# Performance work log

Measured on AMD Instinct MI355X. Metric: run time of the kernel, lower is better.

Reference implementation:

```python
import jax, jax.numpy as jnp
import numpy as np

B, SQ, SK, D = 8, 4096, 4096, 64


def setup_inputs() -> dict:
    key = jax.random.key(0)
    k1, k2, k3 = jax.random.split(key, 3)
    x1 = jax.random.normal(k1, (B, SQ, D), dtype=jnp.float32)   # queries
    x2 = jax.random.normal(k2, (B, SK, D), dtype=jnp.float32)   # keys
    x3 = jax.random.normal(k3, (B, SK, D), dtype=jnp.float32)   # values
    x4 = 0                                                      # dropout p (static, 0 => deterministic)
    x5 = jnp.ones((1,), dtype=jnp.float32)                      # scale divisor
    return {"x1": x1, "x2": x2, "x3": x3, "x4": x4, "x5": x5}


def reference(x1, x2, x3, x4, x5):
    # scores: [B, Sq, Sk]
    scores = jnp.einsum("bqd,bkd->bqk", x1, x2) / x5
    attn = jax.nn.softmax(scores, axis=-1)
    p = float(x4)  # static python scalar
    if p > 0.0:
        mask = jax.random.bernoulli(jax.random.key(42), 1.0 - p, attn.shape)
        attn = attn * mask.astype(attn.dtype) / (1.0 - p)
    # out: [B, Sq, D]
    return jnp.einsum("bqk,bkd->bqd", attn, x3)
```

## Files before the change

kernel.cpp:

```cpp
#include <hip/hip_runtime.h>


typedef _Float16 f16x8 __attribute__((ext_vector_type(8)));
typedef _Float16 f16x4 __attribute__((ext_vector_type(4)));
typedef __fp16   h16x2 __attribute__((ext_vector_type(2)));
typedef float    f32x4 __attribute__((ext_vector_type(4)));

constexpr int kB  = 8;
constexpr int kSQ = 4096;
constexpr int kSK = 4096;
constexpr int kD  = 64;
constexpr int BQ  = 64;
constexpr int BK  = 64;
constexpr int LDK = kD + 8;
constexpr int LDV = BK + 8;
constexpr int LDP = BK + 8;

static __device__ __forceinline__ f16x4 pack4(float a, float b, float c, float d) {
    h16x2 p0 = __builtin_amdgcn_cvt_pkrtz(a, b);
    h16x2 p1 = __builtin_amdgcn_cvt_pkrtz(c, d);
    f16x4 r;
    r[0] = (_Float16)p0[0]; r[1] = (_Float16)p0[1];
    r[2] = (_Float16)p1[0]; r[3] = (_Float16)p1[1];
    return r;
}

__global__ __launch_bounds__(256, 2)
void fattn_kernel(const float* __restrict__ Qg,
                  const float* __restrict__ Kg,
                  const float* __restrict__ Vg,
                  const float* __restrict__ sdiv,
                  float* __restrict__ Og)
{
    __shared__ __align__(16) _Float16 sK[2][BK][LDK];
    __shared__ __align__(16) _Float16 sV[2][kD][LDV];
    __shared__ __align__(16) _Float16 sP[4][16][LDP];

    const int tid  = threadIdx.x;
    const int w    = tid >> 6;
    const int lane = tid & 63;
    const int l16  = lane & 15;
    const int quad = lane >> 4;

    const int b  = blockIdx.y;
    const int qb = blockIdx.x * BQ;

    const float inv_scale = 1.0f / sdiv[0];

    const float* Qb = Qg + ((size_t)b * kSQ + qb) * kD;
    const float* Kb = Kg + (size_t)b * kSK * kD;
    const float* Vb = Vg + (size_t)b * kSK * kD;

    f16x8 qf[2];
    {
        const float* qrow = Qb + (size_t)(w * 16 + l16) * kD;
#pragma unroll
        for (int ks = 0; ks < 2; ++ks) {
            const float4 a = *(const float4*)(qrow + ks * 32 + quad * 8);
            const float4 c = *(const float4*)(qrow + ks * 32 + quad * 8 + 4);
            f16x4 lo = pack4(a.x * inv_scale, a.y * inv_scale, a.z * inv_scale, a.w * inv_scale);
            f16x4 hi = pack4(c.x * inv_scale, c.y * inv_scale, c.z * inv_scale, c.w * inv_scale);
            f16x8 f;
            f[0] = lo[0]; f[1] = lo[1]; f[2] = lo[2]; f[3] = lo[3];
            f[4] = hi[0]; f[5] = hi[1]; f[6] = hi[2]; f[7] = hi[3];
            qf[ks] = f;
        }
    }

    const int kp0 = 2 * ((0 * 256 + tid) >> 4), cb0 = ((0 * 256 + tid) & 15) * 4;
    const int kp1 = 2 * ((1 * 256 + tid) >> 4), cb1 = ((1 * 256 + tid) & 15) * 4;
    const int kq  = tid >> 4;
    const int fq  = tid & 15;
    const int kqs = (kq ^ (fq & 14)) * 4;

    float4 rk[2][2];
    float4 rv[4];

    auto load_tile = [&](int kt) {
        const float* Kt = Kb + (size_t)kt * BK * kD;
        const float* Vt = Vb + (size_t)kt * BK * kD;
        rk[0][0] = *(const float4*)(Kt + (kp0 + 0) * kD + cb0);
        rk[0][1] = *(const float4*)(Kt + (kp0 + 1) * kD + cb0);
        rk[1][0] = *(const float4*)(Kt + (kp1 + 0) * kD + cb1);
        rk[1][1] = *(const float4*)(Kt + (kp1 + 1) * kD + cb1);
#pragma unroll
        for (int r = 0; r < 4; ++r)
            rv[r] = *(const float4*)(Vt + (4 * kq + r) * kD + 4 * fq);
    };

    auto write_tile = [&](int buf) {
        *(f16x4*)&sK[buf][kp0 + 0][cb0] = pack4(rk[0][0].x, rk[0][0].y, rk[0][0].z, rk[0][0].w);
        *(f16x4*)&sK[buf][kp0 + 1][cb0] = pack4(rk[0][1].x, rk[0][1].y, rk[0][1].z, rk[0][1].w);
        *(f16x4*)&sK[buf][kp1 + 0][cb1] = pack4(rk[1][0].x, rk[1][0].y, rk[1][0].z, rk[1][0].w);
        *(f16x4*)&sK[buf][kp1 + 1][cb1] = pack4(rk[1][1].x, rk[1][1].y, rk[1][1].z, rk[1][1].w);
        const float vx[4][4] = {
            {rv[0].x, rv[0].y, rv[0].z, rv[0].w},
            {rv[1].x, rv[1].y, rv[1].z, rv[1].w},
            {rv[2].x, rv[2].y, rv[2].z, rv[2].w},
            {rv[3].x, rv[3].y, rv[3].z, rv[3].w}};
#pragma unroll
        for (int j = 0; j < 4; ++j)
            *(f16x4*)&sV[buf][4 * fq + j][kqs] =
                pack4(vx[0][j], vx[1][j], vx[2][j], vx[3][j]);
    };

    f32x4 o[4];
    float m_i = -1e30f, l_i = 0.0f;
#pragma unroll
    for (int dt = 0; dt < 4; ++dt)
#pragma unroll
        for (int r = 0; r < 4; ++r) o[dt][r] = 0.0f;

    load_tile(0);
    write_tile(0);
    __syncthreads();

    const int nIter = kSK / BK;
    for (int kt = 0; kt < nIter; ++kt) {
        const int buf = kt & 1;
        const bool more = (kt + 1 < nIter);
        if (more) load_tile(kt + 1);

        f32x4 s[4];
#pragma unroll
        for (int nt = 0; nt < 4; ++nt) {
            const f16x8 kf0 = *(const f16x8*)&sK[buf][nt * 16 + l16][quad * 8];
            const f16x8 kf1 = *(const f16x8*)&sK[buf][nt * 16 + l16][32 + quad * 8];
            f32x4 acc;
#pragma unroll
            for (int r = 0; r < 4; ++r) acc[r] = 0.0f;
            acc = __builtin_amdgcn_mfma_f32_16x16x32_f16(kf0, qf[0], acc, 0, 0, 0);
            acc = __builtin_amdgcn_mfma_f32_16x16x32_f16(kf1, qf[1], acc, 0, 0, 0);
            s[nt] = acc;
        }

        float rm = s[0][0];
#pragma unroll
        for (int nt = 0; nt < 4; ++nt)
#pragma unroll
            for (int r = 0; r < 4; ++r) rm = fmaxf(rm, s[nt][r]);
        rm = fmaxf(rm, __shfl_xor(rm, 16, 64));
        rm = fmaxf(rm, __shfl_xor(rm, 32, 64));
        const float mnew = fmaxf(m_i, rm);
        const float alpha = __expf(m_i - mnew);
        m_i = mnew;
        float rs = 0.0f;
#pragma unroll
        for (int nt = 0; nt < 4; ++nt)
#pragma unroll
            for (int r = 0; r < 4; ++r) {
                const float p = __expf(s[nt][r] - mnew);
                s[nt][r] = p;
                rs += p;
            }
        rs += __shfl_xor(rs, 16, 64);
        rs += __shfl_xor(rs, 32, 64);
        l_i = l_i * alpha + rs;
#pragma unroll
        for (int dt = 0; dt < 4; ++dt)
#pragma unroll
            for (int r = 0; r < 4; ++r) o[dt][r] *= alpha;

#pragma unroll
        for (int nt = 0; nt < 4; ++nt)
            *(f16x4*)&sP[w][l16][nt * 16 + quad * 4] =
                pack4(s[nt][0], s[nt][1], s[nt][2], s[nt][3]);

        const f16x8 pf0 = *(const f16x8*)&sP[w][l16][quad * 8];
        const f16x8 pf1 = *(const f16x8*)&sP[w][l16][32 + quad * 8];
#pragma unroll
        for (int dt = 0; dt < 4; ++dt) {
            const int f   = dt * 16 + l16;
            const int sw  = (f >> 2) & 14;
            const f16x8 vf0 = *(const f16x8*)&sV[buf][f][((2 * quad) ^ sw) * 4];
            const f16x8 vf1 = *(const f16x8*)&sV[buf][f][((8 + 2 * quad) ^ sw) * 4];
            o[dt] = __builtin_amdgcn_mfma_f32_16x16x32_f16(vf0, pf0, o[dt], 0, 0, 0);
            o[dt] = __builtin_amdgcn_mfma_f32_16x16x32_f16(vf1, pf1, o[dt], 0, 0, 0);
        }

        if (more) write_tile(buf ^ 1);
        __syncthreads();
    }

    float* Ob = Og + ((size_t)b * kSQ + qb) * kD;
    const int qrow = w * 16 + l16;
    const float linv = 1.0f / l_i;
#pragma unroll
    for (int dt = 0; dt < 4; ++dt) {
        float4 st4;
        st4.x = o[dt][0] * linv;
        st4.y = o[dt][1] * linv;
        st4.z = o[dt][2] * linv;
        st4.w = o[dt][3] * linv;
        *(float4*)&Ob[(size_t)qrow * kD + dt * 16 + quad * 4] = st4;
    }
}

extern "C" void kernel_launch(void* const* d_in, const int* in_sizes, int n_in,
                              void* d_out, int out_size, void* d_ws, size_t ws_size,
                              hipStream_t stream) {
    const float* Q    = (const float*)d_in[0];
    const float* K    = (const float*)d_in[1];
    const float* V    = (const float*)d_in[2];
    const float* sdiv = (const float*)d_in[4];
    float* O = (float*)d_out;

    dim3 grid(kSQ / BQ, kB);
    fattn_kernel<<<grid, dim3(256), 0, stream>>>(Q, K, V, sdiv, O);
}
```

Measured before the change: 149.1 us.

## Double query tile per block and split keys across two partial passes

Each wave now handles two 16-row query tiles (BQ=128), so every K/V tile staged in LDS is reused across twice as many query rows, halving K/V global traffic and conversion work per query. To keep the grid size unchanged, the key sequence is split into two halves along a new grid dimension. Each half writes unnormalized partial outputs plus per-row max and sum to workspace, and a second combine kernel merges them. This adds a workspace round trip of about 16 MB each way, an extra launch, and higher register pressure from doubled accumulators.

```diff
diff --git a/kernel.cpp b/kernel.cpp
--- a/kernel.cpp
+++ b/kernel.cpp
@@ -10,11 +10,14 @@
 constexpr int kSQ = 4096;
 constexpr int kSK = 4096;
 constexpr int kD  = 64;
-constexpr int BQ  = 64;
+constexpr int KSPLIT = 2;
+constexpr int SKH = kSK / KSPLIT;
+constexpr int BQ  = 128;
 constexpr int BK  = 64;
 constexpr int LDK = kD + 8;
 constexpr int LDV = BK + 8;
 constexpr int LDP = BK + 8;
+constexpr size_t APART = (size_t)kB * kSQ * kD;
 
 static __device__ __forceinline__ f16x4 pack4(float a, float b, float c, float d) {
     h16x2 p0 = __builtin_amdgcn_cvt_pkrtz(a, b);
@@ -26,15 +29,16 @@
 }
 
 __global__ __launch_bounds__(256, 2)
-void fattn_kernel(const float* __restrict__ Qg,
-                  const float* __restrict__ Kg,
-                  const float* __restrict__ Vg,
-                  const float* __restrict__ sdiv,
-                  float* __restrict__ Og)
+void fattn_partial(const float* __restrict__ Qg,
+                   const float* __restrict__ Kg,
+                   const float* __restrict__ Vg,
+                   const float* __restrict__ sdiv,
+                   float* __restrict__ Ap,
+                   float2* __restrict__ MLp)
 {
     __shared__ __align__(16) _Float16 sK[2][BK][LDK];
     __shared__ __align__(16) _Float16 sV[2][kD][LDV];
-    __shared__ __align__(16) _Float16 sP[4][16][LDP];
+    __shared__ __align__(16) _Float16 sP[4][2][16][LDP];
 
     const int tid  = threadIdx.x;
     const int w    = tid >> 6;
@@ -44,26 +48,28 @@
 
     const int b  = blockIdx.y;
     const int qb = blockIdx.x * BQ;
+    const int ks = blockIdx.z;
 
     const float inv_scale = 1.0f / sdiv[0];
 
     const float* Qb = Qg + ((size_t)b * kSQ + qb) * kD;
-    const float* Kb = Kg + (size_t)b * kSK * kD;
-    const float* Vb = Vg + (size_t)b * kSK * kD;
-
-    f16x8 qf[2];
-    {
-        const float* qrow = Qb + (size_t)(w * 16 + l16) * kD;
-#pragma unroll
-        for (int ks = 0; ks < 2; ++ks) {
-            const float4 a = *(const float4*)(qrow + ks * 32 + quad * 8);
-            const float4 c = *(const float4*)(qrow + ks * 32 + quad * 8 + 4);
+    const float* Kb = Kg + ((size_t)b * kSK + (size_t)ks * SKH) * kD;
+    const float* Vb = Vg + ((size_t)b * kSK + (size_t)ks * SKH) * kD;
+
+    f16x8 qf[2][2];
+#pragma unroll
+    for (int mt = 0; mt < 2; ++mt) {
+        const float* qrow = Qb + (size_t)(w * 32 + mt * 16 + l16) * kD;
+#pragma unroll
+        for (int kk = 0; kk < 2; ++kk) {
+            const float4 a = *(const float4*)(qrow + kk * 32 + quad * 8);
+            const float4 c = *(const float4*)(qrow + kk * 32 + quad * 8 + 4);
             f16x4 lo = pack4(a.x * inv_scale, a.y * inv_scale, a.z * inv_scale, a.w * inv_scale);
             f16x4 hi = pack4(c.x * inv_scale, c.y * inv_scale, c.z * inv_scale, c.w * inv_scale);
             f16x8 f;
             f[0] = lo[0]; f[1] = lo[1]; f[2] = lo[2]; f[3] = lo[3];
             f[4] = hi[0]; f[5] = hi[1]; f[6] = hi[2]; f[7] = hi[3];
-            qf[ks] = f;
+            qf[mt][kk] = f;
         }
     }
 
@@ -104,96 +110,137 @@
                 pack4(vx[0][j], vx[1][j], vx[2][j], vx[3][j]);
     };
 
-    f32x4 o[4];
-    float m_i = -1e30f, l_i = 0.0f;
-#pragma unroll
-    for (int dt = 0; dt < 4; ++dt)
-#pragma unroll
-        for (int r = 0; r < 4; ++r) o[dt][r] = 0.0f;
+    f32x4 o[2][4];
+    float m_i[2] = {-1e30f, -1e30f}, l_i[2] = {0.0f, 0.0f};
+#pragma unroll
+    for (int mt = 0; mt < 2; ++mt)
+#pragma unroll
+        for (int dt = 0; dt < 4; ++dt)
+#pragma unroll
+            for (int r = 0; r < 4; ++r) o[mt][dt][r] = 0.0f;
 
     load_tile(0);
     write_tile(0);
     __syncthreads();
 
-    const int nIter = kSK / BK;
+    const int nIter = SKH / BK;
     for (int kt = 0; kt < nIter; ++kt) {
         const int buf = kt & 1;
         const bool more = (kt + 1 < nIter);
         if (more) load_tile(kt + 1);
 
-        f32x4 s[4];
+        f32x4 s[2][4];
 #pragma unroll
         for (int nt = 0; nt < 4; ++nt) {
             const f16x8 kf0 = *(const f16x8*)&sK[buf][nt * 16 + l16][quad * 8];
             const f16x8 kf1 = *(const f16x8*)&sK[buf][nt * 16 + l16][32 + quad * 8];
-            f32x4 acc;
-#pragma unroll
-            for (int r = 0; r < 4; ++r) acc[r] = 0.0f;
-            acc = __builtin_amdgcn_mfma_f32_16x16x32_f16(kf0, qf[0], acc, 0, 0, 0);
-            acc = __builtin_amdgcn_mfma_f32_16x16x32_f16(kf1, qf[1], acc, 0, 0, 0);
-            s[nt] = acc;
-        }
-
-        float rm = s[0][0];
-#pragma unroll
-        for (int nt = 0; nt < 4; ++nt)
-#pragma unroll
-            for (int r = 0; r < 4; ++r) rm = fmaxf(rm, s[nt][r]);
-        rm = fmaxf(rm, __shfl_xor(rm, 16, 64));
-        rm = fmaxf(rm, __shfl_xor(rm, 32, 64));
-        const float mnew = fmaxf(m_i, rm);
-        const float alpha = __expf(m_i - mnew);
-        m_i = mnew;
-        float rs = 0.0f;
-#pragma unroll
-        for (int nt = 0; nt < 4; ++nt)
-#pragma unroll
-            for (int r = 0; r < 4; ++r) {
-                const float p = __expf(s[nt][r] - mnew);
-                s[nt][r] = p;
-                rs += p;
+#pragma unroll
+            for (int mt = 0; mt < 2; ++mt) {
+                f32x4 acc;
+#pragma unroll
+                for (int r = 0; r < 4; ++r) acc[r] = 0.0f;
+                acc = __builtin_amdgcn_mfma_f32_16x16x32_f16(kf0, qf[mt][0], acc, 0, 0, 0);
+                acc = __builtin_amdgcn_mfma_f32_16x16x32_f16(kf1, qf[mt][1], acc, 0, 0, 0);
+                s[mt][nt] = acc;
             }
-        rs += __shfl_xor(rs, 16, 64);
-        rs += __shfl_xor(rs, 32, 64);
-        l_i = l_i * alpha + rs;
-#pragma unroll
-        for (int dt = 0; dt < 4; ++dt)
-#pragma unroll
-            for (int r = 0; r < 4; ++r) o[dt][r] *= alpha;
-
-#pragma unroll
-        for (int nt = 0; nt < 4; ++nt)
-            *(f16x4*)&sP[w][l16][nt * 16 + quad * 4] =
-                pack4(s[nt][0], s[nt][1], s[nt][2], s[nt][3]);
-
-        const f16x8 pf0 = *(const f16x8*)&sP[w][l16][quad * 8];
-        const f16x8 pf1 = *(const f16x8*)&sP[w][l16][32 + quad * 8];
+        }
+
+#pragma unroll
+        for (int mt = 0; mt < 2; ++mt) {
+            float rm = s[mt][0][0];
+#pragma unroll
+            for (int nt = 0; nt < 4; ++nt)
+#pragma unroll
+                for (int r = 0; r < 4; ++r) rm = fmaxf(rm, s[mt][nt][r]);
+            rm = fmaxf(rm, __shfl_xor(rm, 16, 64));
+            rm = fmaxf(rm, __shfl_xor(rm, 32, 64));
+            const float mnew = fmaxf(m_i[mt], rm);
+            const float alpha = __expf(m_i[mt] - mnew);
+            m_i[mt] = mnew;
+            float rs = 0.0f;
+#pragma unroll
+            for (int nt = 0; nt < 4; ++nt)
+#pragma unroll
+                for (int r = 0; r < 4; ++r) {
+                    const float p = __expf(s[mt][nt][r] - mnew);
+                    s[mt][nt][r] = p;
+                    rs += p;
+                }
+            rs += __shfl_xor(rs, 16, 64);
+            rs += __shfl_xor(rs, 32, 64);
+            l_i[mt] = l_i[mt] * alpha + rs;
+#pragma unroll
+            for (int dt = 0; dt < 4; ++dt)
+#pragma unroll
+                for (int r = 0; r < 4; ++r) o[mt][dt][r] *= alpha;
+#pragma unroll
+            for (int nt = 0; nt < 4; ++nt)
+                *(f16x4*)&sP[w][mt][l16][nt * 16 + quad * 4] =
+                    pack4(s[mt][nt][0], s[mt][nt][1], s[mt][nt][2], s[mt][nt][3]);
+        }
+
+        const f16x8 pfa0 = *(const f16x8*)&sP[w][0][l16][quad * 8];
+        const f16x8 pfa1 = *(const f16x8*)&sP[w][0][l16][32 + quad * 8];
+        const f16x8 pfb0 = *(const f16x8*)&sP[w][1][l16][quad * 8];
+        const f16x8 pfb1 = *(const f16x8*)&sP[w][1][l16][32 + quad * 8];
 #pragma unroll
         for (int dt = 0; dt < 4; ++dt) {
-            const int f   = dt * 16 + l16;
-            const int sw  = (f >> 2) & 14;
+            const int f  = dt * 16 + l16;
+            const int sw = (f >> 2) & 14;
             const f16x8 vf0 = *(const f16x8*)&sV[buf][f][((2 * quad) ^ sw) * 4];
             const f16x8 vf1 = *(const f16x8*)&sV[buf][f][((8 + 2 * quad) ^ sw) * 4];
-            o[dt] = __builtin_amdgcn_mfma_f32_16x16x32_f16(vf0, pf0, o[dt], 0, 0, 0);
-            o[dt] = __builtin_amdgcn_mfma_f32_16x16x32_f16(vf1, pf1, o[dt], 0, 0, 0);
+            o[0][dt] = __builtin_amdgcn_mfma_f32_16x16x32_f16(vf0, pfa0, o[0][dt], 0, 0, 0);
+            o[0][dt] = __builtin_amdgcn_mfma_f32_16x16x32_f16(vf1, pfa1, o[0][dt], 0, 0, 0);
+            o[1][dt] = __builtin_amdgcn_mfma_f32_16x16x32_f16(vf0, pfb0, o[1][dt], 0, 0, 0);
+            o[1][dt] = __builtin_amdgcn_mfma_f32_16x16x32_f16(vf1, pfb1, o[1][dt], 0, 0, 0);
         }
 
         if (more) write_tile(buf ^ 1);
         __syncthreads();
     }
 
-    float* Ob = Og + ((size_t)b * kSQ + qb) * kD;
-    const int qrow = w * 16 + l16;
-    const float linv = 1.0f / l_i;
-#pragma unroll
-    for (int dt = 0; dt < 4; ++dt) {
-        float4 st4;
-        st4.x = o[dt][0] * linv;
-        st4.y = o[dt][1] * linv;
-        st4.z = o[dt][2] * linv;
-        st4.w = o[dt][3] * linv;
-        *(float4*)&Ob[(size_t)qrow * kD + dt * 16 + quad * 4] = st4;
+    float* Ab = Ap + (size_t)ks * APART + ((size_t)b * kSQ + qb) * kD;
+    float2* MLb = MLp + (size_t)ks * kB * kSQ + (size_t)b * kSQ + qb;
+#pragma unroll
+    for (int mt = 0; mt < 2; ++mt) {
+        const int row = w * 32 + mt * 16 + l16;
+#pragma unroll
+        for (int dt = 0; dt < 4; ++dt) {
+            float4 st4;
+            st4.x = o[mt][dt][0];
+            st4.y = o[mt][dt][1];
+            st4.z = o[mt][dt][2];
+            st4.w = o[mt][dt][3];
+            *(float4*)&Ab[(size_t)row * kD + dt * 16 + quad * 4] = st4;
+        }
+        if (quad == 0) MLb[row] = make_float2(m_i[mt], l_i[mt]);
     }
+}
+
+__global__ __launch_bounds__(256)
+void fattn_combine(const float* __restrict__ Ap,
+                   const float2* __restrict__ MLp,
+                   float* __restrict__ Og)
+{
+    const int idx = blockIdx.x * 256 + threadIdx.x;
+    const int r = idx >> 4;
+    const int c = (idx & 15) * 4;
+
+    const float2 ml0 = MLp[r];
+    const float2 ml1 = MLp[kB * kSQ + r];
+    const float m = fmaxf(ml0.x, ml1.x);
+    const float e0 = __expf(ml0.x - m);
+    const float e1 = __expf(ml1.x - m);
+    const float inv = 1.0f / (e0 * ml0.y + e1 * ml1.y);
+
+    const float4 a0 = *(const float4*)&Ap[(size_t)r * kD + c];
+    const float4 a1 = *(const float4*)&Ap[APART + (size_t)r * kD + c];
+    float4 res;
+    res.x = (e0 * a0.x + e1 * a1.x) * inv;
+    res.y = (e0 * a0.y + e1 * a1.y) * inv;
+    res.z = (e0 * a0.z + e1 * a1.z) * inv;
+    res.w = (e0 * a0.w + e1 * a1.w) * inv;
+    *(float4*)&Og[(size_t)r * kD + c] = res;
 }
 
 extern "C" void kernel_launch(void* const* d_in, const int* in_sizes, int n_in,
@@ -205,6 +252,10 @@
     const float* sdiv = (const float*)d_in[4];
     float* O = (float*)d_out;
 
-    dim3 grid(kSQ / BQ, kB);
-    fattn_kernel<<<grid, dim3(256), 0, stream>>>(Q, K, V, sdiv, O);
-}
+    float*  Ap  = (float*)d_ws;
+    float2* MLp = (float2*)(Ap + KSPLIT * APART);
+
+    dim3 grid(kSQ / BQ, kB, KSPLIT);
+    fattn_partial<<<grid, dim3(256), 0, stream>>>(Q, K, V, sdiv, Ap, MLp);
+    fattn_combine<<<dim3(kB * kSQ * kD / (256 * 4)), dim3(256), 0, stream>>>(Ap, MLp, O);
+}
```

After: 153.9 us. +3.2%, slower.
